# Kernel tuning notes

Measured on AMD Instinct MI355X. Metric: run time of the kernel, lower is better.

The kernel has to match this reference:

```python
import jax, jax.numpy as jnp
import numpy as np

NUM_HEADS = 16
D_MODEL = 1024
D_K = D_MODEL // NUM_HEADS


def setup_inputs() -> dict:
    key = jax.random.key(0)
    ks = jax.random.split(key, 11)
    B, S = 2, 2048
    s = 1.0 / np.sqrt(D_MODEL)
    return {
        "Q": jax.random.normal(ks[0], (B, S, D_MODEL), jnp.float32),
        "K": jax.random.normal(ks[1], (B, S, D_MODEL), jnp.float32),
        "V": jax.random.normal(ks[2], (B, S, D_MODEL), jnp.float32),
        "Wq": jax.random.normal(ks[3], (D_MODEL, D_MODEL), jnp.float32) * s,
        "bq": jnp.zeros((D_MODEL,), jnp.float32),
        "Wk": jax.random.normal(ks[4], (D_MODEL, D_MODEL), jnp.float32) * s,
        "bk": jnp.zeros((D_MODEL,), jnp.float32),
        "Wv": jax.random.normal(ks[5], (D_MODEL, D_MODEL), jnp.float32) * s,
        "bv": jnp.zeros((D_MODEL,), jnp.float32),
        "Wo": jax.random.normal(ks[6], (D_MODEL, D_MODEL), jnp.float32) * s,
        "bo": jnp.zeros((D_MODEL,), jnp.float32),
    }


def _split_heads(x):
    B, S, _ = x.shape
    return x.reshape(B, S, NUM_HEADS, D_K).transpose(0, 2, 1, 3)  # (B,H,S,Dk)


def reference(Q, K, V, Wq, bq, Wk, bk, Wv, bv, Wo, bo):
    q = _split_heads(Q @ Wq + bq)
    k = _split_heads(K @ Wk + bk)
    v = _split_heads(V @ Wv + bv)
    scores = jnp.einsum("bhqd,bhkd->bhqk", q, k) / jnp.sqrt(jnp.asarray(D_K, q.dtype))
    attn = jax.nn.softmax(scores, axis=-1)
    out = jnp.einsum("bhqk,bhkd->bhqd", attn, v)  # (B,H,S,Dk)
    B, H, S, Dk = out.shape
    combined = out.transpose(0, 2, 1, 3).reshape(B, S, H * Dk)
    return combined @ Wo + bo
```

## Files before the change

kernel.cpp:

```cpp
#include <hip/hip_runtime.h>
#include <stdint.h>

#define DM   1024
#define NH   16
#define DKH  64
#define SEQ  2048
#define NB   2

typedef __attribute__((ext_vector_type(8))) short  frag8;
typedef __attribute__((ext_vector_type(4))) short  short4v;
typedef __attribute__((ext_vector_type(8))) short  short8v;
typedef __attribute__((ext_vector_type(4))) float  f32x4;

__device__ __forceinline__ unsigned short f2bf(float x){
  unsigned u = __float_as_uint(x);
  u += 0x7fffu + ((u >> 16) & 1u);
  return (unsigned short)(u >> 16);
}

#define GLOAD16(GP, LP) __builtin_amdgcn_global_load_lds( \
    (__attribute__((address_space(1))) void*)(GP), \
    (__attribute__((address_space(3))) void*)(LP), 16, 0, 0)


__global__ __launch_bounds__(256) void cast_qkv(const float* __restrict__ Q,
                                                const float* __restrict__ K,
                                                const float* __restrict__ V,
                                                short* __restrict__ dst){
  const int z = blockIdx.z;
  const float* src = (z == 0) ? Q : (z == 1 ? K : V);
  const int i = (blockIdx.x * 256 + threadIdx.x) * 4;
  float4 f = *(const float4*)(src + i);
  short4v s;
  s.x = (short)f2bf(f.x); s.y = (short)f2bf(f.y);
  s.z = (short)f2bf(f.z); s.w = (short)f2bf(f.w);
  *(short4v*)(dst + (long)z * (SEQ*NB*DM) + i) = s;
}

__global__ __launch_bounds__(256) void wtrans(const float* __restrict__ Wq,
                                              const float* __restrict__ Wk,
                                              const float* __restrict__ Wv,
                                              const float* __restrict__ Wo,
                                              short* __restrict__ wt){
  const int z = blockIdx.z;
  const float* W = (z == 0) ? Wq : (z == 1 ? Wk : (z == 2 ? Wv : Wo));
  short* out = wt + (long)z * (DM*DM);
  __shared__ float t[32][33];
  const int n0 = blockIdx.x * 32, k0 = blockIdx.y * 32;
  const int c = threadIdx.x & 31, r0 = threadIdx.x >> 5;
#pragma unroll
  for (int i = 0; i < 4; ++i){
    int r = r0 + i * 8;
    t[r][c] = W[(k0 + r) * DM + n0 + c];
  }
  __syncthreads();
#pragma unroll
  for (int i = 0; i < 4; ++i){
    int r = r0 + i * 8;
    out[(n0 + r) * DM + k0 + c] = (short)f2bf(t[c][r]);
  }
}

__device__ __forceinline__ void store_out(short* p, float v){ *p = (short)f2bf(v); }
__device__ __forceinline__ void store_out(float* p, float v){ *p = v; }

template<typename OT>
__global__ __launch_bounds__(256) void gemm_bt(const short* __restrict__ Abase, long Astride,
                                               const short* __restrict__ Btbase, long Btstride,
                                               const float* __restrict__ bias0,
                                               const float* __restrict__ bias1,
                                               const float* __restrict__ bias2,
                                               OT* __restrict__ Cbase, long Cstride,
                                               float qscale){
  const int z = blockIdx.z;
  const short* A  = Abase + (long)z * Astride;
  const short* Bt = Btbase + (long)z * Btstride;
  OT* C = Cbase + (long)z * Cstride;
  const float* bias = (z == 0) ? bias0 : (z == 1 ? bias1 : bias2);
  const float scale = (z == 0) ? qscale : 1.0f;
  const int KD = DM, ND = DM;

  __shared__ __align__(16) short As[128 * 64];
  __shared__ __align__(16) short Bs[128 * 64];

  const int tid = threadIdx.x;
  const int w = tid >> 6, lane = tid & 63, l15 = lane & 15, quad = lane >> 4;
  const int wy = w >> 1, wx = w & 1;
  const int bm = blockIdx.x * 128, bn = blockIdx.y * 128;
  const int lrow = lane >> 3;
  const int lcolsw = (((lane & 7) ^ lrow) & 7) * 8;

  f32x4 acc[4][4] = {};

  for (int kt = 0; kt < KD; kt += 64){
#pragma unroll
    for (int i = 0; i < 4; ++i){
      int j = w * 4 + i;
      GLOAD16(A  + (bm + j * 8 + lrow) * KD + kt + lcolsw, &As[j * 512]);
      GLOAD16(Bt + (bn + j * 8 + lrow) * KD + kt + lcolsw, &Bs[j * 512]);
    }
    __syncthreads();
#pragma unroll
    for (int ks = 0; ks < 2; ++ks){
      frag8 af[4], bf_[4];
#pragma unroll
      for (int mt = 0; mt < 4; ++mt)
        af[mt] = *(const frag8*)&As[(wy * 64 + mt * 16 + l15) * 64 +
                                    (((ks * 4 + quad) ^ (l15 & 7)) * 8)];
#pragma unroll
      for (int nt = 0; nt < 4; ++nt)
        bf_[nt] = *(const frag8*)&Bs[(wx * 64 + nt * 16 + l15) * 64 +
                                     (((ks * 4 + quad) ^ (l15 & 7)) * 8)];
#pragma unroll
      for (int mt = 0; mt < 4; ++mt)
#pragma unroll
        for (int nt = 0; nt < 4; ++nt)
          acc[mt][nt] = __builtin_amdgcn_mfma_f32_16x16x32_bf16(af[mt], bf_[nt], acc[mt][nt], 0, 0, 0);
    }
    __syncthreads();
  }

#pragma unroll
  for (int mt = 0; mt < 4; ++mt){
#pragma unroll
    for (int r = 0; r < 4; ++r){
      int m = bm + wy * 64 + mt * 16 + quad * 4 + r;
#pragma unroll
      for (int nt = 0; nt < 4; ++nt){
        int n = bn + wx * 64 + nt * 16 + l15;
        float v = (acc[mt][nt][r] + bias[n]) * scale;
        store_out(&C[(long)m * ND + n], v);
      }
    }
  }
}

template<typename OT>
__global__ __launch_bounds__(256) void gemm64_bt(const short* __restrict__ A,
                                                 const short* __restrict__ Bt,
                                                 const float* __restrict__ bias,
                                                 OT* __restrict__ C,
                                                 float scale){
  const int KD = DM, ND = DM;
  __shared__ __align__(16) short As[64 * 64];
  __shared__ __align__(16) short Bs[128 * 64];
  const int tid = threadIdx.x;
  const int w = tid >> 6, lane = tid & 63, l15 = lane & 15, quad = lane >> 4;
  const int wy = w >> 1, wx = w & 1;
  const int bm = blockIdx.x * 64, bn = blockIdx.y * 128;
  const int lrow = lane >> 3;
  const int lcolsw = (((lane & 7) ^ lrow) & 7) * 8;
  f32x4 acc[2][4] = {};

  for (int kt = 0; kt < KD; kt += 64){
#pragma unroll
    for (int i = 0; i < 2; ++i){
      int j = w * 2 + i;
      GLOAD16(A + (bm + j * 8 + lrow) * KD + kt + lcolsw, &As[j * 512]);
    }
#pragma unroll
    for (int i = 0; i < 4; ++i){
      int j = w * 4 + i;
      GLOAD16(Bt + (bn + j * 8 + lrow) * KD + kt + lcolsw, &Bs[j * 512]);
    }
    __syncthreads();
#pragma unroll
    for (int ks = 0; ks < 2; ++ks){
      frag8 af[2], bf_[4];
#pragma unroll
      for (int mt = 0; mt < 2; ++mt)
        af[mt] = *(const frag8*)&As[(wy * 32 + mt * 16 + l15) * 64 +
                                    (((ks * 4 + quad) ^ (l15 & 7)) * 8)];
#pragma unroll
      for (int nt = 0; nt < 4; ++nt)
        bf_[nt] = *(const frag8*)&Bs[(wx * 64 + nt * 16 + l15) * 64 +
                                     (((ks * 4 + quad) ^ (l15 & 7)) * 8)];
#pragma unroll
      for (int mt = 0; mt < 2; ++mt)
#pragma unroll
        for (int nt = 0; nt < 4; ++nt)
          acc[mt][nt] = __builtin_amdgcn_mfma_f32_16x16x32_bf16(af[mt], bf_[nt], acc[mt][nt], 0, 0, 0);
    }
    __syncthreads();
  }

#pragma unroll
  for (int mt = 0; mt < 2; ++mt){
#pragma unroll
    for (int r = 0; r < 4; ++r){
      int m = bm + wy * 32 + mt * 16 + quad * 4 + r;
#pragma unroll
      for (int nt = 0; nt < 4; ++nt){
        int n = bn + wx * 64 + nt * 16 + l15;
        store_out(&C[(long)m * ND + n], (acc[mt][nt][r] + bias[n]) * scale);
      }
    }
  }
}

__global__ __launch_bounds__(256) void vtrans(const short* __restrict__ v,
                                              short* __restrict__ vt){
  const int bh = blockIdx.y;
  const int b = bh >> 4, h = bh & 15;
  const int s0 = blockIdx.x * 64;
  __shared__ short tT[64][66];
  const short* vb = v + ((long)(b * SEQ + s0)) * DM + h * DKH;
  for (int j = threadIdx.x; j < 512; j += 256){
    int row = j >> 3, off = (j & 7) * 8;
    short8v d = *(const short8v*)(vb + row * DM + off);
#pragma unroll
    for (int e = 0; e < 8; ++e) tT[off + e][row] = d[e];
  }
  __syncthreads();
  short* out = vt + (long)bh * (DKH * SEQ) + s0;
  for (int j = threadIdx.x; j < 512; j += 256){
    int dr = j >> 3, soff = (j & 7) * 8;
    short8v o;
#pragma unroll
    for (int e = 0; e < 8; ++e) o[e] = tT[dr][soff + e];
    *(short8v*)(out + dr * SEQ + soff) = o;
  }
}

__global__ __launch_bounds__(256) void flash(const short* __restrict__ q,
                                             const short* __restrict__ k,
                                             const short* __restrict__ vt,
                                             short* __restrict__ comb){
  const int bh = blockIdx.y;
  const int b = bh >> 4, h = bh & 15;
  const int q0 = blockIdx.x * 64;
  const int tid = threadIdx.x;
  const int w = tid >> 6, lane = tid & 63, l15 = lane & 15, quad = lane >> 4;

  __shared__ __align__(16) short Ks[64 * 64];
  __shared__ __align__(16) short Vs[64 * 64];
  __shared__ __align__(16) short Ps[4][16 * 64];

  frag8 aq[2];
  const short* qb = q + ((long)(b * SEQ + q0 + w * 16)) * DM + h * DKH;
#pragma unroll
  for (int ks = 0; ks < 2; ++ks)
    aq[ks] = *(const frag8*)(qb + l15 * DM + ks * 32 + quad * 8);

  frag8 ones;
#pragma unroll
  for (int e = 0; e < 8; ++e) ones[e] = (short)0x3F80;

  f32x4 O[4] = {};
  f32x4 Lacc = {0.f, 0.f, 0.f, 0.f};

  const short* kb  = k + ((long)b * SEQ) * DM + h * DKH;
  const short* vtb = vt + (long)bh * (DKH * SEQ);
  const int lrow8 = lane >> 3;
  const int lcolsw = (((lane & 7) ^ lrow8) & 7) * 8;

  for (int kt = 0; kt < SEQ / 64; ++kt){
#pragma unroll
    for (int i = 0; i < 2; ++i){
      int jj = w * 2 + i;
      GLOAD16(kb + (kt * 64 + jj * 8 + lrow8) * DM + lcolsw, &Ks[jj * 512]);
      GLOAD16(vtb + (jj * 8 + lrow8) * SEQ + kt * 64 + lcolsw, &Vs[jj * 512]);
    }
    __syncthreads();

    f32x4 sc[4];
#pragma unroll
    for (int nt = 0; nt < 4; ++nt) sc[nt] = (f32x4){0.f, 0.f, 0.f, 0.f};
#pragma unroll
    for (int ks = 0; ks < 2; ++ks){
      frag8 bk_[4];
#pragma unroll
      for (int nt = 0; nt < 4; ++nt)
        bk_[nt] = *(const frag8*)&Ks[(nt * 16 + l15) * 64 +
                                     (((ks * 4 + quad) ^ (l15 & 7)) * 8)];
#pragma unroll
      for (int nt = 0; nt < 4; ++nt)
        sc[nt] = __builtin_amdgcn_mfma_f32_16x16x32_bf16(aq[ks], bk_[nt], sc[nt], 0, 0, 0);
    }

#pragma unroll
    for (int nt = 0; nt < 4; ++nt){
#pragma unroll
      for (int r = 0; r < 4; ++r){
        float p = __expf(sc[nt][r]);
        unsigned u = (__float_as_uint(p) + 0x8000u) >> 16;
        int row = quad * 4 + r;
        Ps[w][row * 64 + (((nt * 2 + (l15 >> 3)) ^ (row & 7)) * 8) + (l15 & 7)] = (short)u;
      }
    }

#pragma unroll
    for (int ch = 0; ch < 2; ++ch){
      frag8 bv_[4];
#pragma unroll
      for (int nt = 0; nt < 4; ++nt)
        bv_[nt] = *(const frag8*)&Vs[(nt * 16 + l15) * 64 +
                                     (((ch * 4 + quad) ^ (l15 & 7)) * 8)];
      frag8 ap = *(const frag8*)&Ps[w][l15 * 64 + (((ch * 4 + quad) ^ (l15 & 7)) * 8)];
#pragma unroll
      for (int nt = 0; nt < 4; ++nt)
        O[nt] = __builtin_amdgcn_mfma_f32_16x16x32_bf16(ap, bv_[nt], O[nt], 0, 0, 0);
      Lacc = __builtin_amdgcn_mfma_f32_16x16x32_bf16(ap, ones, Lacc, 0, 0, 0);
    }
    __syncthreads();
  }

  short* ob = comb + ((long)(b * SEQ + q0 + w * 16)) * DM + h * DKH;
#pragma unroll
  for (int r = 0; r < 4; ++r){
    float inv = 1.f / Lacc[r];
#pragma unroll
    for (int nt = 0; nt < 4; ++nt)
      ob[(quad * 4 + r) * DM + nt * 16 + l15] = (short)f2bf(O[nt][r] * inv);
  }
}

extern "C" void kernel_launch(void* const* d_in, const int* in_sizes, int n_in,
                              void* d_out, int out_size, void* d_ws, size_t ws_size,
                              hipStream_t stream){
  const float* Q  = (const float*)d_in[0];
  const float* K  = (const float*)d_in[1];
  const float* V  = (const float*)d_in[2];
  const float* Wq = (const float*)d_in[3];
  const float* bq = (const float*)d_in[4];
  const float* Wk = (const float*)d_in[5];
  const float* bk = (const float*)d_in[6];
  const float* Wv = (const float*)d_in[7];
  const float* bv = (const float*)d_in[8];
  const float* Wo = (const float*)d_in[9];
  const float* bo = (const float*)d_in[10];
  float* out = (float*)d_out;

  const long TEN = (long)NB * SEQ * DM;
  const long WEL = (long)DM * DM;
  short* ws   = (short*)d_ws;
  short* xc   = ws;
  short* wt   = xc + 3 * TEN;
  short* qkv  = wt + 4 * WEL;
  short* vtr  = qkv + 3 * TEN;
  short* comb = vtr + TEN;

  cast_qkv<<<dim3(4096, 1, 3), 256, 0, stream>>>(Q, K, V, xc);
  wtrans<<<dim3(32, 32, 4), 256, 0, stream>>>(Wq, Wk, Wv, Wo, wt);
  gemm_bt<short><<<dim3(32, 8, 3), 256, 0, stream>>>(xc, TEN, wt, WEL, bq, bk, bv,
                                                     qkv, TEN, 0.125f);
  vtrans<<<dim3(32, 32), 256, 0, stream>>>(qkv + 2 * TEN, vtr);
  flash<<<dim3(32, 32), 256, 0, stream>>>(qkv, qkv + TEN, vtr, comb);
  gemm64_bt<float><<<dim3(64, 8), 256, 0, stream>>>(comb, wt + 3 * WEL, bo, out, 1.0f);
  (void)in_sizes; (void)n_in; (void)out_size; (void)ws_size;
}
```

Baseline: 248.4 us.

## Keep attention probabilities in registers via transposed QK^T MFMA, drop LDS P staging

Computes the score tile transposed (K as the A operand, Q as the B operand) so each lane's accumulator layout matches the A-operand layout of a 16x16x16 bf16 MFMA. The exponentiated probabilities then feed straight into the PV and row-sum MFMAs from registers, removing the per-wave LDS write/read round trip and the Ps shared buffer. In exchange it uses the smaller-K 16x16x16 MFMA, so the PV product issues twice as many MFMA instructions and twice as many narrower 8-byte V loads from LDS.

```diff
diff --git a/kernel.cpp b/kernel.cpp
--- a/kernel.cpp
+++ b/kernel.cpp
@@ -8,6 +8,7 @@
 #define NB   2
 
 typedef __attribute__((ext_vector_type(8))) short  frag8;
+typedef __attribute__((ext_vector_type(4))) short  frag4;
 typedef __attribute__((ext_vector_type(4))) short  short4v;
 typedef __attribute__((ext_vector_type(8))) short  short8v;
 typedef __attribute__((ext_vector_type(4))) float  f32x4;
@@ -234,7 +235,6 @@
 
   __shared__ __align__(16) short Ks[64 * 64];
   __shared__ __align__(16) short Vs[64 * 64];
-  __shared__ __align__(16) short Ps[4][16 * 64];
 
   frag8 aq[2];
   const short* qb = q + ((long)(b * SEQ + q0 + w * 16)) * DM + h * DKH;
@@ -242,9 +242,9 @@
   for (int ks = 0; ks < 2; ++ks)
     aq[ks] = *(const frag8*)(qb + l15 * DM + ks * 32 + quad * 8);
 
-  frag8 ones;
-#pragma unroll
-  for (int e = 0; e < 8; ++e) ones[e] = (short)0x3F80;
+  frag4 ones4;
+#pragma unroll
+  for (int e = 0; e < 4; ++e) ones4[e] = (short)0x3F80;
 
   f32x4 O[4] = {};
   f32x4 Lacc = {0.f, 0.f, 0.f, 0.f};
@@ -263,44 +263,39 @@
     }
     __syncthreads();
 
-    f32x4 sc[4];
-#pragma unroll
-    for (int nt = 0; nt < 4; ++nt) sc[nt] = (f32x4){0.f, 0.f, 0.f, 0.f};
+    f32x4 scT[4];
+#pragma unroll
+    for (int nt = 0; nt < 4; ++nt) scT[nt] = (f32x4){0.f, 0.f, 0.f, 0.f};
 #pragma unroll
     for (int ks = 0; ks < 2; ++ks){
-      frag8 bk_[4];
-#pragma unroll
-      for (int nt = 0; nt < 4; ++nt)
-        bk_[nt] = *(const frag8*)&Ks[(nt * 16 + l15) * 64 +
-                                     (((ks * 4 + quad) ^ (l15 & 7)) * 8)];
-#pragma unroll
-      for (int nt = 0; nt < 4; ++nt)
-        sc[nt] = __builtin_amdgcn_mfma_f32_16x16x32_bf16(aq[ks], bk_[nt], sc[nt], 0, 0, 0);
-    }
-
+#pragma unroll
+      for (int nt = 0; nt < 4; ++nt){
+        frag8 ak = *(const frag8*)&Ks[(nt * 16 + l15) * 64 +
+                                      (((ks * 4 + quad) ^ (l15 & 7)) * 8)];
+        scT[nt] = __builtin_amdgcn_mfma_f32_16x16x32_bf16(ak, aq[ks], scT[nt], 0, 0, 0);
+      }
+    }
+
+    frag4 ap[4];
 #pragma unroll
     for (int nt = 0; nt < 4; ++nt){
 #pragma unroll
       for (int r = 0; r < 4; ++r){
-        float p = __expf(sc[nt][r]);
-        unsigned u = (__float_as_uint(p) + 0x8000u) >> 16;
-        int row = quad * 4 + r;
-        Ps[w][row * 64 + (((nt * 2 + (l15 >> 3)) ^ (row & 7)) * 8) + (l15 & 7)] = (short)u;
-      }
-    }
-
-#pragma unroll
-    for (int ch = 0; ch < 2; ++ch){
-      frag8 bv_[4];
-#pragma unroll
-      for (int nt = 0; nt < 4; ++nt)
-        bv_[nt] = *(const frag8*)&Vs[(nt * 16 + l15) * 64 +
-                                     (((ch * 4 + quad) ^ (l15 & 7)) * 8)];
-      frag8 ap = *(const frag8*)&Ps[w][l15 * 64 + (((ch * 4 + quad) ^ (l15 & 7)) * 8)];
-#pragma unroll
-      for (int nt = 0; nt < 4; ++nt)
-        O[nt] = __builtin_amdgcn_mfma_f32_16x16x32_bf16(ap, bv_[nt], O[nt], 0, 0, 0);
-      Lacc = __builtin_amdgcn_mfma_f32_16x16x32_bf16(ap, ones, Lacc, 0, 0, 0);
+        unsigned u = (__float_as_uint(__expf(scT[nt][r])) + 0x8000u) >> 16;
+        ap[nt][r] = (short)u;
+      }
+    }
+
+#pragma unroll
+    for (int nt = 0; nt < 4; ++nt){
+#pragma unroll
+      for (int dt = 0; dt < 4; ++dt){
+        frag4 bv4 = *(const frag4*)&Vs[(dt * 16 + l15) * 64 +
+                                       (((nt * 2 + (quad >> 1)) ^ (l15 & 7)) * 8) +
+                                       (quad & 1) * 4];
+        O[dt] = __builtin_amdgcn_mfma_f32_16x16x16bf16_1k(ap[nt], bv4, O[dt], 0, 0, 0);
+      }
+      Lacc = __builtin_amdgcn_mfma_f32_16x16x16bf16_1k(ap[nt], ones4, Lacc, 0, 0, 0);
     }
     __syncthreads();
   }
```

Measured after the change: 248.3 us. Within noise of the previous version (-0.1%).
